# Kernel tuning notes

Hardware: AMD Instinct MI355X
Metric: run time of the kernel (lower is better)

The kernel has to match this reference:

```python
import jax, jax.numpy as jnp
import numpy as np

H = 1024        # hidden_size
NH = 16         # num_attention_heads
HD = H // NH    # attention_head_size = 64
EPS = 1e-12


def setup_inputs() -> dict:
    key = jax.random.key(0)
    ks = jax.random.split(key, 12)
    B, S = 2, 2048
    s = 0.02
    return {
        "hidden_states": jax.random.normal(ks[0], (B, S, H), jnp.float32),
        "attention_mask": jnp.zeros((B, 1, 1, S), jnp.float32),
        "Wq": jax.random.normal(ks[1], (H, H), jnp.float32) * s,
        "bq": jnp.zeros((H,), jnp.float32),
        "Wk": jax.random.normal(ks[2], (H, H), jnp.float32) * s,
        "bk": jnp.zeros((H,), jnp.float32),
        "Wv": jax.random.normal(ks[3], (H, H), jnp.float32) * s,
        "bv": jnp.zeros((H,), jnp.float32),
        "Wd": jax.random.normal(ks[4], (H, H), jnp.float32) * s,
        "bd": jnp.zeros((H,), jnp.float32),
        "ln_gamma": jnp.ones((H,), jnp.float32),
        "ln_beta": jnp.zeros((H,), jnp.float32),
    }


def _split_heads(x):
    # [B,S,H] -> [B,NH,S,HD]
    B, S, _ = x.shape
    return x.reshape(B, S, NH, HD).transpose(0, 2, 1, 3)


def reference(hidden_states, attention_mask, Wq, bq, Wk, bk, Wv, bv, Wd, bd, ln_gamma, ln_beta):
    q = _split_heads(hidden_states @ Wq.T + bq)
    k = _split_heads(hidden_states @ Wk.T + bk)
    v = _split_heads(hidden_states @ Wv.T + bv)

    scores = jnp.einsum("bhqd,bhkd->bhqk", q, k) / jnp.sqrt(jnp.float32(HD))
    scores = scores + attention_mask
    probs = jax.nn.softmax(scores, axis=-1)  # attention dropout p=0

    ctx = jnp.einsum("bhqk,bhkd->bhqd", probs, v)
    B, _, S, _ = ctx.shape
    ctx = ctx.transpose(0, 2, 1, 3).reshape(B, S, H)

    proj = ctx @ Wd.T + bd  # output dropout p=0
    x = hidden_states + proj
    mu = jnp.mean(x, axis=-1, keepdims=True)
    var = jnp.mean(jnp.square(x - mu), axis=-1, keepdims=True)
    out = (x - mu) * jax.lax.rsqrt(var + EPS) * ln_gamma + ln_beta
    return out
```

## Files before the change

kernel.cpp:

```cpp
#include <hip/hip_runtime.h>

typedef unsigned short u16;
typedef unsigned int u32;
typedef __attribute__((ext_vector_type(4))) unsigned short u16x4;
typedef __attribute__((ext_vector_type(8))) unsigned short u16x8;
typedef __attribute__((ext_vector_type(8))) __bf16 bf16x8;
typedef __attribute__((ext_vector_type(4))) float f32x4;

#define S_LEN 2048
#define HDIM 1024
#define NHEAD 16
#define HD 64
#define MTOK 4096
#define QKV_STRIDE 4194304
#define LOG2E 1.44269504089f
#define QKSCL (0.125f * 1.44269504089f)

__device__ __forceinline__ float bf2f(u16 h) {
    unsigned u = ((unsigned)h) << 16;
    return __builtin_bit_cast(float, u);
}
__device__ __forceinline__ u16 f2bf(float f) {
    return __builtin_bit_cast(u16, (__bf16)f);
}
__device__ __forceinline__ bf16x8 as_bf16(u16x8 u) {
    union { u16x8 a; bf16x8 b; } c; c.a = u; return c.b;
}
__device__ __forceinline__ void gld_lds16(const u16* g, u16* l) {
    __builtin_amdgcn_global_load_lds((const __attribute__((address_space(1))) u16*)g,
                                     (__attribute__((address_space(3))) u16*)l, 16, 0, 0);
}

__device__ __forceinline__ void cast4(const float* __restrict__ s, u16* __restrict__ d, int i) {
    f32x4 v = *(const f32x4*)(s + (size_t)i * 4);
    u16x4 o;
    o[0] = f2bf(v[0]); o[1] = f2bf(v[1]); o[2] = f2bf(v[2]); o[3] = f2bf(v[3]);
    *(u16x4*)(d + (size_t)i * 4) = o;
}

__global__ __launch_bounds__(256) void prep(const float* __restrict__ hs,
                                            const float* __restrict__ Wq, const float* __restrict__ Wk,
                                            const float* __restrict__ Wv, const float* __restrict__ Wd,
                                            const float* __restrict__ bq, const float* __restrict__ bk,
                                            const float* __restrict__ bv,
                                            u16* __restrict__ hsb, u16* __restrict__ wqkvb,
                                            u16* __restrict__ wdb, float* __restrict__ b3) {
    int bid = blockIdx.x, tid = threadIdx.x;
    if (bid < 4096) {
        cast4(hs, hsb, bid * 256 + tid);
    } else if (bid < 5120) {
        cast4(Wq, wqkvb, (bid - 4096) * 256 + tid);
    } else if (bid < 6144) {
        cast4(Wk, wqkvb + HDIM * HDIM, (bid - 5120) * 256 + tid);
    } else if (bid < 7168) {
        cast4(Wv, wqkvb + 2 * HDIM * HDIM, (bid - 6144) * 256 + tid);
    } else if (bid < 8192) {
        cast4(Wd, wdb, (bid - 7168) * 256 + tid);
    } else {
        int i = (bid - 8192) * 256 + tid;
        if (i < 3072) b3[i] = (i < 1024) ? bq[i] : (i < 2048) ? bk[i - 1024] : bv[i - 2048];
    }
}

__global__ __launch_bounds__(256, 3) void gemm_qkv(const u16* __restrict__ A, const u16* __restrict__ Bw,
                                                   const float* __restrict__ bias,
                                                   u16* __restrict__ outb, u16* __restrict__ vtout) {
    __shared__ alignas(16) u16 As[2][128 * 32];
    __shared__ alignas(16) u16 Bs[2][128 * 32];
    const int Kd = 1024;
    const int tid = threadIdx.x;
    const int wave = tid >> 6, lane = tid & 63;
    const int l15 = lane & 15, l4 = lane >> 4;
    const int m0 = blockIdx.y * 128, n0 = blockIdx.x * 128;
    const int wm = wave >> 1, wn = wave & 1;

    const int cc0 = wave * 2;
    const int srow = lane >> 2;
    const int sco = (lane & 3) * 8;

    f32x4 acc[4][4];
#pragma unroll
    for (int i = 0; i < 4; i++)
#pragma unroll
        for (int j = 0; j < 4; j++) acc[i][j] = (f32x4){0.f, 0.f, 0.f, 0.f};

    auto STAGE = [&](int k0, int buf) {
#pragma unroll
        for (int i = 0; i < 2; i++) {
            int cc = cc0 + i;
            int row = cc * 16 + srow;
            gld_lds16(A + (size_t)(m0 + row) * Kd + k0 + sco, &As[buf][cc * 512]);
            gld_lds16(Bw + (size_t)(n0 + row) * Kd + k0 + sco, &Bs[buf][cc * 512]);
        }
    };

    const int nt = Kd >> 5;
    STAGE(0, 0);
    for (int t = 0; t < nt; ++t) {
        __builtin_amdgcn_s_barrier();
        if (t + 1 < nt) {
            STAGE((t + 1) << 5, (t + 1) & 1);
            asm volatile("s_waitcnt vmcnt(4)" ::: "memory");
        } else {
            asm volatile("s_waitcnt vmcnt(0)" ::: "memory");
        }
        __builtin_amdgcn_s_barrier();
        const u16* as = &As[t & 1][0];
        const u16* bs = &Bs[t & 1][0];
        bf16x8 af[4], bf[4];
#pragma unroll
        for (int x = 0; x < 4; x++) {
            af[x] = as_bf16(*(const u16x8*)&as[(wm * 64 + x * 16 + l15) * 32 + l4 * 8]);
            bf[x] = as_bf16(*(const u16x8*)&bs[(wn * 64 + x * 16 + l15) * 32 + l4 * 8]);
        }
        __builtin_amdgcn_s_setprio(1);
#pragma unroll
        for (int mi = 0; mi < 4; mi++)
#pragma unroll
            for (int nj = 0; nj < 4; nj++)
                acc[mi][nj] = __builtin_amdgcn_mfma_f32_16x16x32_bf16(af[mi], bf[nj], acc[mi][nj], 0, 0, 0);
        __builtin_amdgcn_s_setprio(0);
    }

#pragma unroll
    for (int mi = 0; mi < 4; mi++) {
#pragma unroll
        for (int nj = 0; nj < 4; nj++) {
            int coln = n0 + wn * 64 + nj * 16 + l15;
            float bv_ = bias[coln];
            int rowb = m0 + wm * 64 + mi * 16 + l4 * 4;
            int which = coln >> 10, nn = coln & 1023;
            int hh = nn >> 6, dd = nn & 63;
            int bb = rowb >> 11, ss = rowb & 2047;
            if (which < 2) {
#pragma unroll
                for (int r = 0; r < 4; r++)
                    outb[(size_t)which * QKV_STRIDE + ((size_t)((bb << 4) + hh) * S_LEN + ss + r) * HD + dd] =
                        f2bf(acc[mi][nj][r] + bv_);
            } else {
                u16x4 o;
#pragma unroll
                for (int r = 0; r < 4; r++) o[r] = f2bf(acc[mi][nj][r] + bv_);
                *(u16x4*)(vtout + ((size_t)((bb << 4) + hh) * HD + dd) * S_LEN + ss) = o;
            }
        }
    }
}

__global__ __launch_bounds__(256, 3) void gemm_proj(const u16* __restrict__ A, const u16* __restrict__ Bw,
                                                    const float* __restrict__ bias,
                                                    u16* __restrict__ outb, int Nd, int Kd) {
    __shared__ alignas(16) u16 As[2][128 * 32];
    __shared__ alignas(16) u16 Bs[2][128 * 32];
    const int tid = threadIdx.x;
    const int wave = tid >> 6, lane = tid & 63;
    const int l15 = lane & 15, l4 = lane >> 4;
    const int m0 = blockIdx.y * 128, n0 = blockIdx.x * 128;
    const int wm = wave >> 1, wn = wave & 1;

    const int cc0 = wave * 2;
    const int srow = lane >> 2;
    const int sco = (lane & 3) * 8;

    f32x4 acc[4][4];
#pragma unroll
    for (int i = 0; i < 4; i++)
#pragma unroll
        for (int j = 0; j < 4; j++) acc[i][j] = (f32x4){0.f, 0.f, 0.f, 0.f};

    auto STAGE = [&](int k0, int buf) {
#pragma unroll
        for (int i = 0; i < 2; i++) {
            int cc = cc0 + i;
            int row = cc * 16 + srow;
            gld_lds16(A + (size_t)(m0 + row) * Kd + k0 + sco, &As[buf][cc * 512]);
            gld_lds16(Bw + (size_t)(n0 + row) * Kd + k0 + sco, &Bs[buf][cc * 512]);
        }
    };

    const int nt = Kd >> 5;
    STAGE(0, 0);
    for (int t = 0; t < nt; ++t) {
        __builtin_amdgcn_s_barrier();
        if (t + 1 < nt) {
            STAGE((t + 1) << 5, (t + 1) & 1);
            asm volatile("s_waitcnt vmcnt(4)" ::: "memory");
        } else {
            asm volatile("s_waitcnt vmcnt(0)" ::: "memory");
        }
        __builtin_amdgcn_s_barrier();
        const u16* as = &As[t & 1][0];
        const u16* bs = &Bs[t & 1][0];
        bf16x8 af[4], bf[4];
#pragma unroll
        for (int x = 0; x < 4; x++) {
            af[x] = as_bf16(*(const u16x8*)&as[(wm * 64 + x * 16 + l15) * 32 + l4 * 8]);
            bf[x] = as_bf16(*(const u16x8*)&bs[(wn * 64 + x * 16 + l15) * 32 + l4 * 8]);
        }
        __builtin_amdgcn_s_setprio(1);
#pragma unroll
        for (int mi = 0; mi < 4; mi++)
#pragma unroll
            for (int nj = 0; nj < 4; nj++)
                acc[mi][nj] = __builtin_amdgcn_mfma_f32_16x16x32_bf16(af[mi], bf[nj], acc[mi][nj], 0, 0, 0);
        __builtin_amdgcn_s_setprio(0);
    }

#pragma unroll
    for (int mi = 0; mi < 4; mi++) {
#pragma unroll
        for (int nj = 0; nj < 4; nj++) {
            int coln = n0 + wn * 64 + nj * 16 + l15;
            float bv_ = bias[coln];
            int rowb = m0 + wm * 64 + mi * 16 + l4 * 4;
#pragma unroll
            for (int r = 0; r < 4; r++)
                outb[(size_t)(rowb + r) * Nd + coln] = f2bf(acc[mi][nj][r] + bv_);
        }
    }
}

__global__ __launch_bounds__(512, 4) void flash_attn9(const u16* __restrict__ qkv,
                                                      const u16* __restrict__ vt,
                                                      const float* __restrict__ amask,
                                                      u16* __restrict__ ctx) {
    __shared__ alignas(16) u16 Kb[3][4096];
    __shared__ alignas(16) u16 Vb[3][4096];
    __shared__ alignas(16) u16 Pl[8][1024];
    __shared__ u16 Mlb[2048];

    const int tid = threadIdx.x;
    const int wave = tid >> 6, lane = tid & 63;
    const int l15 = lane & 15, l4 = lane >> 4;
    const int lid = blockIdx.x;
    const int idx = lid >> 3;
    const int bh = (lid & 7) * 4 + (idx >> 4);
    const int qx = idx & 15;
    const int b = bh >> 4, h = bh & 15;
    const int qr0 = qx * 128 + wave * 16;

    const u16* qh = qkv + (size_t)bh * (S_LEN * HD);
    const u16* kh = qh + QKV_STRIDE;
    const u16* vth = vt + (size_t)bh * (S_LEN * HD);
    u16* pw = &Pl[wave][0];

    {
        f32x4 m = *(const f32x4*)(amask + (size_t)b * S_LEN + tid * 4);
        u16x4 mm;
#pragma unroll
        for (int j = 0; j < 4; j++) mm[j] = f2bf(m[j] * LOG2E);
        *(u16x4*)&Mlb[tid * 4] = mm;
    }

    bf16x8 qf[2];
#pragma unroll
    for (int ks = 0; ks < 2; ks++)
        qf[ks] = as_bf16(*(const u16x8*)(qh + (size_t)(qr0 + l15) * HD + ks * 32 + l4 * 8));

    __syncthreads();

    const int srow = lane >> 3;
    const int schunk = (lane & 7) ^ srow;
    const int krow = wave * 8 + srow;
    const u16* ksrc = kh + (size_t)krow * HD + schunk * 8;
    const u16* vsrc = vth + (size_t)krow * S_LEN + schunk * 8;

    f32x4 acc_o[4];
    float l_run = 0.f;
#pragma unroll
    for (int x = 0; x < 4; x++) acc_o[x] = (f32x4){0.f, 0.f, 0.f, 0.f};

    auto STAGE = [&](int T, int buf) {
        gld_lds16(ksrc + (size_t)T * 64 * HD, &Kb[buf][wave * 512]);
        gld_lds16(vsrc + T * 64, &Vb[buf][wave * 512]);
    };

    auto tile = [&](int t, int buf) {
        const u16* kb = &Kb[buf][0];
        const u16* vb = &Vb[buf][0];
        f32x4 accs[4];
#pragma unroll
        for (int nj = 0; nj < 4; nj++) accs[nj] = (f32x4){0.f, 0.f, 0.f, 0.f};
        __builtin_amdgcn_s_setprio(1);
#pragma unroll
        for (int ks = 0; ks < 2; ks++) {
            bf16x8 kf[4];
#pragma unroll
            for (int nj = 0; nj < 4; nj++) {
                int n = nj * 16 + l15;
                kf[nj] = as_bf16(*(const u16x8*)&kb[n * 64 + ((ks * 32 + l4 * 8) ^ ((n & 7) << 3))]);
            }
#pragma unroll
            for (int nj = 0; nj < 4; nj++)
                accs[nj] = __builtin_amdgcn_mfma_f32_16x16x32_bf16(kf[nj], qf[ks], accs[nj], 0, 0, 0);
        }
        __builtin_amdgcn_s_setprio(0);
        const int kv0 = t * 64;
        const int rsw = (l15 & 7) << 3;
#pragma unroll
        for (int nj = 0; nj < 4; nj++) {
            u16x4 mraw = *(const u16x4*)&Mlb[kv0 + nj * 16 + l4 * 4];
            u16x4 o;
#pragma unroll
            for (int r = 0; r < 4; r++) {
                float p = __builtin_amdgcn_exp2f(accs[nj][r] * QKSCL + bf2f(mraw[r]));
                l_run += p;
                o[r] = f2bf(p);
            }
            *(u16x4*)&pw[l15 * 64 + ((nj * 16 + l4 * 4) ^ rsw)] = o;
        }
        __builtin_amdgcn_s_setprio(1);
#pragma unroll
        for (int ks = 0; ks < 2; ks++) {
            int kvoff = ks * 32 + l4 * 8;
            bf16x8 pf = as_bf16(*(const u16x8*)&pw[l15 * 64 + (kvoff ^ rsw)]);
            bf16x8 vf[4];
#pragma unroll
            for (int dj = 0; dj < 4; dj++) {
                int d = dj * 16 + l15;
                vf[dj] = as_bf16(*(const u16x8*)&vb[d * 64 + (kvoff ^ ((d & 7) << 3))]);
            }
#pragma unroll
            for (int dj = 0; dj < 4; dj++)
                acc_o[dj] = __builtin_amdgcn_mfma_f32_16x16x32_bf16(vf[dj], pf, acc_o[dj], 0, 0, 0);
        }
        __builtin_amdgcn_s_setprio(0);
    };

    STAGE(0, 0);
    STAGE(1, 1);
    for (int t = 0; t < 32; ++t) {
        if (t < 31) {
            asm volatile("s_waitcnt vmcnt(2)" ::: "memory");
        } else {
            asm volatile("s_waitcnt vmcnt(0)" ::: "memory");
        }
        __builtin_amdgcn_s_barrier();
        if (t + 2 < 32) STAGE(t + 2, (t + 2) % 3);
        tile(t, t % 3);
    }

    float l = l_run;
    l += __shfl_xor(l, 16);
    l += __shfl_xor(l, 32);
    float inv = 1.0f / l;
    u16* cp = ctx + ((size_t)b * S_LEN + qr0 + l15) * HDIM + h * HD + l4 * 4;
#pragma unroll
    for (int dj = 0; dj < 4; dj++) {
        u16x4 o;
#pragma unroll
        for (int r = 0; r < 4; r++) o[r] = f2bf(acc_o[dj][r] * inv);
        *(u16x4*)(cp + dj * 16) = o;
    }
}

__global__ __launch_bounds__(256) void resid_ln(const float* __restrict__ hs, const u16* __restrict__ proj,
                                                const float* __restrict__ g, const float* __restrict__ be,
                                                float* __restrict__ out) {
    int row = blockIdx.x, tid = threadIdx.x;
    int base = row * HDIM + tid * 4;
    f32x4 a = *(const f32x4*)(hs + base);
    u16x4 pb = *(const u16x4*)(proj + base);
    f32x4 x;
#pragma unroll
    for (int j = 0; j < 4; j++) x[j] = a[j] + bf2f(pb[j]);
    float s = x[0] + x[1] + x[2] + x[3];
    float sq = x[0] * x[0] + x[1] * x[1] + x[2] * x[2] + x[3] * x[3];
#pragma unroll
    for (int m = 1; m < 64; m <<= 1) {
        s += __shfl_xor(s, m);
        sq += __shfl_xor(sq, m);
    }
    __shared__ float red[8];
    int wave = tid >> 6, lane = tid & 63;
    if (lane == 0) { red[wave] = s; red[4 + wave] = sq; }
    __syncthreads();
    s = red[0] + red[1] + red[2] + red[3];
    sq = red[4] + red[5] + red[6] + red[7];
    float mean = s * (1.0f / 1024.0f);
    float var = sq * (1.0f / 1024.0f) - mean * mean;
    float rstd = rsqrtf(fmaxf(var, 0.f) + 1e-12f);
    f32x4 gg = *(const f32x4*)(g + tid * 4);
    f32x4 bb = *(const f32x4*)(be + tid * 4);
    f32x4 o;
#pragma unroll
    for (int j = 0; j < 4; j++) o[j] = (x[j] - mean) * rstd * gg[j] + bb[j];
    *(f32x4*)(out + base) = o;
}

extern "C" void kernel_launch(void* const* d_in, const int* in_sizes, int n_in,
                              void* d_out, int out_size, void* d_ws, size_t ws_size,
                              hipStream_t stream) {
    const float* hs    = (const float*)d_in[0];
    const float* amask = (const float*)d_in[1];
    const float* Wq    = (const float*)d_in[2];
    const float* bq    = (const float*)d_in[3];
    const float* Wk    = (const float*)d_in[4];
    const float* bk    = (const float*)d_in[5];
    const float* Wv    = (const float*)d_in[6];
    const float* bv    = (const float*)d_in[7];
    const float* Wd    = (const float*)d_in[8];
    const float* bd    = (const float*)d_in[9];
    const float* gamma = (const float*)d_in[10];
    const float* beta  = (const float*)d_in[11];

    char* ws = (char*)d_ws;
    u16*   hsb   = (u16*)(ws);
    u16*   Wqkvb = (u16*)(ws + ((size_t)8 << 20));
    u16*   Wdb   = (u16*)(ws + ((size_t)14 << 20));
    u16*   qkv   = (u16*)(ws + ((size_t)16 << 20));
    u16*   vt    = qkv + 2 * (size_t)QKV_STRIDE;
    u16*   ctx   = (u16*)(ws + ((size_t)40 << 20));
    u16*   projb = (u16*)(ws + ((size_t)48 << 20));
    float* b3    = (float*)(ws + ((size_t)64 << 20));

    prep<<<8204, 256, 0, stream>>>(hs, Wq, Wk, Wv, Wd, bq, bk, bv, hsb, Wqkvb, Wdb, b3);

    gemm_qkv<<<dim3(24, 32), 256, 0, stream>>>(hsb, Wqkvb, b3, qkv, vt);

    flash_attn9<<<512, 512, 0, stream>>>(qkv, vt, amask, ctx);

    gemm_proj<<<dim3(8, 32), 256, 0, stream>>>(ctx, Wdb, bd, projb, HDIM, HDIM);

    resid_ln<<<MTOK, 256, 0, stream>>>(hs, projb, gamma, beta, (float*)d_out);
}
```

Baseline: 127.0 us.

## Rewrite attention with 32x32 MFMA, register-resident P, and split-KV wave groups

The attention kernel now uses 32x32x16 MFMA tiles, and each wave processes 64 query rows instead of 16. Each block is split into two wave groups that each handle half the KV sequence, and their partial outputs and row sums are merged through shared memory at the end. The P matrix stays in registers and is rearranged with permlane32 swaps instead of a round trip through LDS. This cuts LDS traffic and K/V reloads per query, at the cost of fewer blocks, higher register pressure, and an extra reduction step.

```diff
diff --git a/kernel.cpp b/kernel.cpp
--- a/kernel.cpp
+++ b/kernel.cpp
@@ -6,6 +6,8 @@
 typedef __attribute__((ext_vector_type(8))) unsigned short u16x8;
 typedef __attribute__((ext_vector_type(8))) __bf16 bf16x8;
 typedef __attribute__((ext_vector_type(4))) float f32x4;
+typedef __attribute__((ext_vector_type(16))) float f32x16;
+typedef __attribute__((ext_vector_type(2))) int i32x2;
 
 #define S_LEN 2048
 #define HDIM 1024
@@ -29,6 +31,20 @@
 __device__ __forceinline__ void gld_lds16(const u16* g, u16* l) {
     __builtin_amdgcn_global_load_lds((const __attribute__((address_space(1))) u16*)g,
                                      (__attribute__((address_space(3))) u16*)l, 16, 0, 0);
+}
+
+__device__ __forceinline__ void pl32swap(u32& a, u32& b) {
+#if __has_builtin(__builtin_amdgcn_permlane32_swap)
+    i32x2 r = __builtin_amdgcn_permlane32_swap((int)a, (int)b, false, false);
+    a = (u32)r[0]; b = (u32)r[1];
+#else
+    u32 as = (u32)__shfl_xor((int)a, 32);
+    u32 bs = (u32)__shfl_xor((int)b, 32);
+    bool hi = (threadIdx.x & 32) != 0;
+    u32 na = hi ? bs : a;
+    u32 nb = hi ? b : as;
+    a = na; b = nb;
+#endif
 }
 
 __device__ __forceinline__ void cast4(const float* __restrict__ s, u16* __restrict__ d, int i) {
@@ -220,29 +236,32 @@
     }
 }
 
-__global__ __launch_bounds__(512, 4) void flash_attn9(const u16* __restrict__ qkv,
-                                                      const u16* __restrict__ vt,
-                                                      const float* __restrict__ amask,
-                                                      u16* __restrict__ ctx) {
-    __shared__ alignas(16) u16 Kb[3][4096];
-    __shared__ alignas(16) u16 Vb[3][4096];
-    __shared__ alignas(16) u16 Pl[8][1024];
-    __shared__ u16 Mlb[2048];
+__global__ __launch_bounds__(512, 2) void flash_attn10(const u16* __restrict__ qkv,
+                                                       const u16* __restrict__ vt,
+                                                       const float* __restrict__ amask,
+                                                       u16* __restrict__ ctx) {
+    __shared__ alignas(16) char smem[102400];
 
     const int tid = threadIdx.x;
     const int wave = tid >> 6, lane = tid & 63;
-    const int l15 = lane & 15, l4 = lane >> 4;
+    const int l31 = lane & 31;
+    const int hi = lane >> 5;
+    const int hi4 = hi * 4;
+    const int g = wave >> 2;
+    const int ws = wave & 3;
+
     const int lid = blockIdx.x;
     const int idx = lid >> 3;
-    const int bh = (lid & 7) * 4 + (idx >> 4);
-    const int qx = idx & 15;
+    const int bh = (lid & 7) * 4 + (idx >> 3);
+    const int qb = idx & 7;
     const int b = bh >> 4, h = bh & 15;
-    const int qr0 = qx * 128 + wave * 16;
+    const int qr0 = qb * 256 + ws * 64;
 
     const u16* qh = qkv + (size_t)bh * (S_LEN * HD);
     const u16* kh = qh + QKV_STRIDE;
     const u16* vth = vt + (size_t)bh * (S_LEN * HD);
-    u16* pw = &Pl[wave][0];
+
+    u16* Mlb = (u16*)(smem + 98304);
 
     {
         f32x4 m = *(const f32x4*)(amask + (size_t)b * S_LEN + tid * 4);
@@ -252,105 +271,163 @@
         *(u16x4*)&Mlb[tid * 4] = mm;
     }
 
-    bf16x8 qf[2];
-#pragma unroll
-    for (int ks = 0; ks < 2; ks++)
-        qf[ks] = as_bf16(*(const u16x8*)(qh + (size_t)(qr0 + l15) * HD + ks * 32 + l4 * 8));
+    bf16x8 qf0[4], qf1[4];
+#pragma unroll
+    for (int s = 0; s < 4; ++s) {
+        qf0[s] = as_bf16(*(const u16x8*)(qh + (size_t)(qr0 + l31) * HD + s * 16 + hi * 8));
+        qf1[s] = as_bf16(*(const u16x8*)(qh + (size_t)(qr0 + 32 + l31) * HD + s * 16 + hi * 8));
+    }
 
     __syncthreads();
 
     const int srow = lane >> 3;
     const int schunk = (lane & 7) ^ srow;
-    const int krow = wave * 8 + srow;
-    const u16* ksrc = kh + (size_t)krow * HD + schunk * 8;
-    const u16* vsrc = vth + (size_t)krow * S_LEN + schunk * 8;
-
-    f32x4 acc_o[4];
-    float l_run = 0.f;
-#pragma unroll
-    for (int x = 0; x < 4; x++) acc_o[x] = (f32x4){0.f, 0.f, 0.f, 0.f};
-
-    auto STAGE = [&](int T, int buf) {
-        gld_lds16(ksrc + (size_t)T * 64 * HD, &Kb[buf][wave * 512]);
-        gld_lds16(vsrc + T * 64, &Vb[buf][wave * 512]);
+    const u16* kss = kh + (size_t)(g * 1024 + ws * 16 + srow) * HD + schunk * 8;
+    const u16* vss = vth + (size_t)(ws * 16 + srow) * S_LEN + g * 1024 + schunk * 8;
+
+    f32x16 oacc00, oacc01, oacc10, oacc11;
+#pragma unroll
+    for (int i = 0; i < 16; ++i) { oacc00[i] = 0.f; oacc01[i] = 0.f; oacc10[i] = 0.f; oacc11[i] = 0.f; }
+    float l_run0 = 0.f, l_run1 = 0.f;
+
+    auto STAGE = [&](int t, int buf) {
+        u16* base = (u16*)(smem + g * 49152 + buf * 16384);
+        u16* kd = base + ws * 1024;
+        u16* vd = base + 4096 + ws * 1024;
+        const u16* ks = kss + (size_t)t * 64 * HD;
+        const u16* vs = vss + t * 64;
+        gld_lds16(ks, kd);
+        gld_lds16(ks + 8 * HD, kd + 512);
+        gld_lds16(vs, vd);
+        gld_lds16(vs + 8 * S_LEN, vd + 512);
     };
 
     auto tile = [&](int t, int buf) {
-        const u16* kb = &Kb[buf][0];
-        const u16* vb = &Vb[buf][0];
-        f32x4 accs[4];
-#pragma unroll
-        for (int nj = 0; nj < 4; nj++) accs[nj] = (f32x4){0.f, 0.f, 0.f, 0.f};
-        __builtin_amdgcn_s_setprio(1);
-#pragma unroll
-        for (int ks = 0; ks < 2; ks++) {
-            bf16x8 kf[4];
-#pragma unroll
-            for (int nj = 0; nj < 4; nj++) {
-                int n = nj * 16 + l15;
-                kf[nj] = as_bf16(*(const u16x8*)&kb[n * 64 + ((ks * 32 + l4 * 8) ^ ((n & 7) << 3))]);
+        const u16* kb = (const u16*)(smem + g * 49152 + buf * 16384);
+        const u16* vb = kb + 4096;
+        const int kv0 = g * 1024 + t * 64;
+#pragma unroll
+        for (int sub = 0; sub < 2; ++sub) {
+            f32x16 acc0, acc1;
+#pragma unroll
+            for (int i = 0; i < 16; ++i) { acc0[i] = 0.f; acc1[i] = 0.f; }
+            const int kvrow = sub * 32 + l31;
+            const int ksw = (kvrow & 7) << 3;
+            __builtin_amdgcn_s_setprio(1);
+#pragma unroll
+            for (int s = 0; s < 4; ++s) {
+                bf16x8 kf = as_bf16(*(const u16x8*)&kb[kvrow * 64 + (((s * 2 + hi) << 3) ^ ksw)]);
+                acc0 = __builtin_amdgcn_mfma_f32_32x32x16_bf16(kf, qf0[s], acc0, 0, 0, 0);
+                acc1 = __builtin_amdgcn_mfma_f32_32x32x16_bf16(kf, qf1[s], acc1, 0, 0, 0);
             }
-#pragma unroll
-            for (int nj = 0; nj < 4; nj++)
-                accs[nj] = __builtin_amdgcn_mfma_f32_16x16x32_bf16(kf[nj], qf[ks], accs[nj], 0, 0, 0);
-        }
-        __builtin_amdgcn_s_setprio(0);
-        const int kv0 = t * 64;
-        const int rsw = (l15 & 7) << 3;
-#pragma unroll
-        for (int nj = 0; nj < 4; nj++) {
-            u16x4 mraw = *(const u16x4*)&Mlb[kv0 + nj * 16 + l4 * 4];
-            u16x4 o;
-#pragma unroll
-            for (int r = 0; r < 4; r++) {
-                float p = __builtin_amdgcn_exp2f(accs[nj][r] * QKSCL + bf2f(mraw[r]));
-                l_run += p;
-                o[r] = f2bf(p);
+            __builtin_amdgcn_s_setprio(0);
+            u32 pw0[8], pw1[8];
+#pragma unroll
+            for (int rg = 0; rg < 4; ++rg) {
+                u16x4 mraw = *(const u16x4*)&Mlb[kv0 + sub * 32 + rg * 8 + hi4];
+#pragma unroll
+                for (int r2 = 0; r2 < 2; ++r2) {
+                    float m0 = bf2f(mraw[r2 * 2]), m1 = bf2f(mraw[r2 * 2 + 1]);
+                    float pa0 = __builtin_amdgcn_exp2f(acc0[rg * 4 + r2 * 2] * QKSCL + m0);
+                    float pb0 = __builtin_amdgcn_exp2f(acc0[rg * 4 + r2 * 2 + 1] * QKSCL + m1);
+                    float pa1 = __builtin_amdgcn_exp2f(acc1[rg * 4 + r2 * 2] * QKSCL + m0);
+                    float pb1 = __builtin_amdgcn_exp2f(acc1[rg * 4 + r2 * 2 + 1] * QKSCL + m1);
+                    l_run0 += pa0 + pb0;
+                    l_run1 += pa1 + pb1;
+                    pw0[rg * 2 + r2] = (u32)f2bf(pa0) | ((u32)f2bf(pb0) << 16);
+                    pw1[rg * 2 + r2] = (u32)f2bf(pa1) | ((u32)f2bf(pb1) << 16);
+                }
             }
-            *(u16x4*)&pw[l15 * 64 + ((nj * 16 + l4 * 4) ^ rsw)] = o;
-        }
-        __builtin_amdgcn_s_setprio(1);
-#pragma unroll
-        for (int ks = 0; ks < 2; ks++) {
-            int kvoff = ks * 32 + l4 * 8;
-            bf16x8 pf = as_bf16(*(const u16x8*)&pw[l15 * 64 + (kvoff ^ rsw)]);
-            bf16x8 vf[4];
-#pragma unroll
-            for (int dj = 0; dj < 4; dj++) {
-                int d = dj * 16 + l15;
-                vf[dj] = as_bf16(*(const u16x8*)&vb[d * 64 + (kvoff ^ ((d & 7) << 3))]);
+            pl32swap(pw0[0], pw0[2]); pl32swap(pw0[1], pw0[3]);
+            pl32swap(pw0[4], pw0[6]); pl32swap(pw0[5], pw0[7]);
+            pl32swap(pw1[0], pw1[2]); pl32swap(pw1[1], pw1[3]);
+            pl32swap(pw1[4], pw1[6]); pl32swap(pw1[5], pw1[7]);
+            union { u32 w[4]; u16x8 v; } u0a, u0b, u1a, u1b;
+            u0a.w[0] = pw0[0]; u0a.w[1] = pw0[1]; u0a.w[2] = pw0[2]; u0a.w[3] = pw0[3];
+            u0b.w[0] = pw0[4]; u0b.w[1] = pw0[5]; u0b.w[2] = pw0[6]; u0b.w[3] = pw0[7];
+            u1a.w[0] = pw1[0]; u1a.w[1] = pw1[1]; u1a.w[2] = pw1[2]; u1a.w[3] = pw1[3];
+            u1b.w[0] = pw1[4]; u1b.w[1] = pw1[5]; u1b.w[2] = pw1[6]; u1b.w[3] = pw1[7];
+            bf16x8 pf0a = as_bf16(u0a.v), pf0b = as_bf16(u0b.v);
+            bf16x8 pf1a = as_bf16(u1a.v), pf1b = as_bf16(u1b.v);
+            __builtin_amdgcn_s_setprio(1);
+            {
+                const int drow0 = l31, dsw0 = (drow0 & 7) << 3;
+                const int drow1 = 32 + l31, dsw1 = (drow1 & 7) << 3;
+                const int c0 = (sub * 4 + hi) << 3;
+                const int c1 = ((sub * 2 + 1) * 2 + hi) << 3;
+                bf16x8 vf;
+                vf = as_bf16(*(const u16x8*)&vb[drow0 * 64 + (c0 ^ dsw0)]);
+                oacc00 = __builtin_amdgcn_mfma_f32_32x32x16_bf16(vf, pf0a, oacc00, 0, 0, 0);
+                oacc10 = __builtin_amdgcn_mfma_f32_32x32x16_bf16(vf, pf1a, oacc10, 0, 0, 0);
+                vf = as_bf16(*(const u16x8*)&vb[drow0 * 64 + (c1 ^ dsw0)]);
+                oacc00 = __builtin_amdgcn_mfma_f32_32x32x16_bf16(vf, pf0b, oacc00, 0, 0, 0);
+                oacc10 = __builtin_amdgcn_mfma_f32_32x32x16_bf16(vf, pf1b, oacc10, 0, 0, 0);
+                vf = as_bf16(*(const u16x8*)&vb[drow1 * 64 + (c0 ^ dsw1)]);
+                oacc01 = __builtin_amdgcn_mfma_f32_32x32x16_bf16(vf, pf0a, oacc01, 0, 0, 0);
+                oacc11 = __builtin_amdgcn_mfma_f32_32x32x16_bf16(vf, pf1a, oacc11, 0, 0, 0);
+                vf = as_bf16(*(const u16x8*)&vb[drow1 * 64 + (c1 ^ dsw1)]);
+                oacc01 = __builtin_amdgcn_mfma_f32_32x32x16_bf16(vf, pf0b, oacc01, 0, 0, 0);
+                oacc11 = __builtin_amdgcn_mfma_f32_32x32x16_bf16(vf, pf1b, oacc11, 0, 0, 0);
             }
-#pragma unroll
-            for (int dj = 0; dj < 4; dj++)
-                acc_o[dj] = __builtin_amdgcn_mfma_f32_16x16x32_bf16(vf[dj], pf, acc_o[dj], 0, 0, 0);
-        }
-        __builtin_amdgcn_s_setprio(0);
+            __builtin_amdgcn_s_setprio(0);
+        }
     };
 
     STAGE(0, 0);
     STAGE(1, 1);
-    for (int t = 0; t < 32; ++t) {
-        if (t < 31) {
-            asm volatile("s_waitcnt vmcnt(2)" ::: "memory");
+    for (int t = 0; t < 16; ++t) {
+        if (t < 15) {
+            asm volatile("s_waitcnt vmcnt(4)" ::: "memory");
         } else {
             asm volatile("s_waitcnt vmcnt(0)" ::: "memory");
         }
         __builtin_amdgcn_s_barrier();
-        if (t + 2 < 32) STAGE(t + 2, (t + 2) % 3);
+        if (t + 2 < 16) STAGE(t + 2, (t + 2) % 3);
         tile(t, t % 3);
     }
 
-    float l = l_run;
-    l += __shfl_xor(l, 16);
-    l += __shfl_xor(l, 32);
-    float inv = 1.0f / l;
-    u16* cp = ctx + ((size_t)b * S_LEN + qr0 + l15) * HDIM + h * HD + l4 * 4;
-#pragma unroll
-    for (int dj = 0; dj < 4; dj++) {
-        u16x4 o;
-#pragma unroll
-        for (int r = 0; r < 4; r++) o[r] = f2bf(acc_o[dj][r] * inv);
-        *(u16x4*)(cp + dj * 16) = o;
+    float l0 = l_run0 + __shfl_xor(l_run0, 32);
+    float l1 = l_run1 + __shfl_xor(l_run1, 32);
+    __syncthreads();
+    float* Oex = (float*)smem;
+    float* lsum = (float*)(smem + 65536);
+    if (g == 1) {
+#pragma unroll
+        for (int rg = 0; rg < 4; ++rg)
+#pragma unroll
+            for (int rr = 0; rr < 4; ++rr) {
+                int dA = hi4 + 8 * rg + rr;
+                int dB = 32 + hi4 + 8 * rg + rr;
+                Oex[ws * 4096 + dA * 64 + l31]      = oacc00[rg * 4 + rr];
+                Oex[ws * 4096 + dB * 64 + l31]      = oacc01[rg * 4 + rr];
+                Oex[ws * 4096 + dA * 64 + 32 + l31] = oacc10[rg * 4 + rr];
+                Oex[ws * 4096 + dB * 64 + 32 + l31] = oacc11[rg * 4 + rr];
+            }
+        if (lane < 32) { lsum[ws * 64 + l31] = l0; lsum[ws * 64 + 32 + l31] = l1; }
+    }
+    __syncthreads();
+    if (g == 0) {
+        float inv0 = 1.0f / (l0 + lsum[ws * 64 + l31]);
+        float inv1 = 1.0f / (l1 + lsum[ws * 64 + 32 + l31]);
+        u16* cp0 = ctx + ((size_t)b * S_LEN + qr0 + l31) * HDIM + h * HD;
+        u16* cp1 = ctx + ((size_t)b * S_LEN + qr0 + 32 + l31) * HDIM + h * HD;
+#pragma unroll
+        for (int rg = 0; rg < 4; ++rg) {
+            u16x4 oA0, oB0, oA1, oB1;
+#pragma unroll
+            for (int rr = 0; rr < 4; ++rr) {
+                int dA = hi4 + 8 * rg + rr;
+                int dB = 32 + hi4 + 8 * rg + rr;
+                oA0[rr] = f2bf((oacc00[rg * 4 + rr] + Oex[ws * 4096 + dA * 64 + l31]) * inv0);
+                oB0[rr] = f2bf((oacc01[rg * 4 + rr] + Oex[ws * 4096 + dB * 64 + l31]) * inv0);
+                oA1[rr] = f2bf((oacc10[rg * 4 + rr] + Oex[ws * 4096 + dA * 64 + 32 + l31]) * inv1);
+                oB1[rr] = f2bf((oacc11[rg * 4 + rr] + Oex[ws * 4096 + dB * 64 + 32 + l31]) * inv1);
+            }
+            *(u16x4*)(cp0 + hi4 + 8 * rg) = oA0;
+            *(u16x4*)(cp0 + 32 + hi4 + 8 * rg) = oB0;
+            *(u16x4*)(cp1 + hi4 + 8 * rg) = oA1;
+            *(u16x4*)(cp1 + 32 + hi4 + 8 * rg) = oB1;
+        }
     }
 }
 
@@ -418,7 +495,7 @@
 
     gemm_qkv<<<dim3(24, 32), 256, 0, stream>>>(hsb, Wqkvb, b3, qkv, vt);
 
-    flash_attn9<<<512, 512, 0, stream>>>(qkv, vt, amask, ctx);
+    flash_attn10<<<256, 512, 0, stream>>>(qkv, vt, amask, ctx);
 
     gemm_proj<<<dim3(8, 32), 256, 0, stream>>>(ctx, Wdb, bd, projb, HDIM, HDIM);
 
```

New measurement: 125.4 us. About the same (-1.3%).
